# Optimization experiments

Measured on AMD Instinct MI355X. Metric: run time of the kernel, lower is better.

## Reference

```python
import jax, jax.numpy as jnp
import numpy as np
from jax.scipy.special import logsumexp

EPSILON = 0.1
MAX_ITERS = 20

B, S, T = 8, 2048, 2048


def setup_inputs() -> dict:
    key = jax.random.key(0)
    k1, k2, k3 = jax.random.split(key, 3)
    cost = jax.random.normal(k1, (B, S, T), dtype=jnp.float32)
    mu = jax.random.uniform(k2, (B, S), dtype=jnp.float32)
    nu = jax.random.uniform(k3, (B, T), dtype=jnp.float32)
    # normalize to probability distributions (realistic OT marginals)
    mu = mu / jnp.sum(mu, axis=-1, keepdims=True)
    nu = nu / jnp.sum(nu, axis=-1, keepdims=True)
    return {"cost": cost, "mu": mu, "nu": nu}


def reference(cost, mu, nu):
    tiny = jnp.finfo(cost.dtype).tiny
    log_mu = jnp.log(jnp.maximum(mu, tiny))          # (B, S)
    log_nu = jnp.log(jnp.maximum(nu, tiny))          # (B, T)
    log_K = -cost / EPSILON                          # (B, S, T)

    def step(carry, _):
        log_u, log_v = carry
        # row update: logsumexp over targets
        log_u = log_mu - logsumexp(log_K + log_v[:, None, :], axis=-1)  # (B, S)
        # col update: logsumexp over sources (equiv. to transpose in torch code)
        log_v = log_nu - logsumexp(log_K + log_u[:, :, None], axis=-2)  # (B, T)
        return (log_u, log_v), None

    init = (jnp.zeros_like(log_mu), jnp.zeros_like(log_nu))
    (log_u, log_v), _ = jax.lax.scan(step, init, None, length=MAX_ITERS)

    log_pi = log_u[:, :, None] + log_K + log_v[:, None, :]  # (B, S, T)
    transport = jnp.exp(log_pi)
    return transport, log_pi
```

## Files before the change

### kernel.cpp

```cpp
#include <hip/hip_runtime.h>
#include <hip/hip_fp16.h>
#include <math.h>

#define BB 8
#define SS 2048
#define TT 2048
#define ITERS 20
#define NEG_EPS_INV -10.0f
#define NWAVE 4
#define NCHUNK 4
#define ROWS 32
#define NTILE (SS / ROWS)
#define TINYF 1.17549435e-38f

typedef float vfloat4 __attribute__((ext_vector_type(4)));

__device__ __forceinline__ float4 fma4v(float a, float4 x, float4 y) {
    return make_float4(fmaf(a, x.x, y.x), fmaf(a, x.y, y.y),
                       fmaf(a, x.z, y.z), fmaf(a, x.w, y.w));
}
__device__ __forceinline__ float4 max4(float4 a, float4 b) {
    return make_float4(fmaxf(a.x, b.x), fmaxf(a.y, b.y),
                       fmaxf(a.z, b.z), fmaxf(a.w, b.w));
}
__device__ __forceinline__ float hmax4(float4 a) {
    return fmaxf(fmaxf(a.x, a.y), fmaxf(a.z, a.w));
}
__device__ __forceinline__ float hsum4(float4 a) {
    return (a.x + a.y) + (a.z + a.w);
}
__device__ __forceinline__ float4 exp4m(float4 x, float m) {
    return make_float4(__expf(x.x - m), __expf(x.y - m),
                       __expf(x.z - m), __expf(x.w - m));
}
__device__ __forceinline__ uint h2u(__half2 h) {
    union { __half2 h; uint u; } c; c.h = h; return c.u;
}
__device__ __forceinline__ __half2 u2h(uint u) {
    union { __half2 h; uint u; } c; c.u = u; return c.h;
}
__device__ __forceinline__ uint2 pack4(float4 f) {
    uint2 r;
    r.x = h2u(__float22half2_rn(make_float2(f.x, f.y)));
    r.y = h2u(__float22half2_rn(make_float2(f.z, f.w)));
    return r;
}
__device__ __forceinline__ float4 unpack4(uint2 u) {
    float2 a = __half22float2(u2h(u.x));
    float2 b = __half22float2(u2h(u.y));
    return make_float4(a.x, a.y, b.x, b.y);
}
__device__ __forceinline__ void nt_store4(float4 v, float* p) {
    vfloat4 x = {v.x, v.y, v.z, v.w};
    __builtin_nontemporal_store(x, reinterpret_cast<vfloat4*>(p));
}

template <bool FIRST>
__global__ __launch_bounds__(256, 3) void sinkhorn_iter(
        const float* __restrict__ cost, uint2* __restrict__ c16,
        const float* __restrict__ mu, const float* __restrict__ nu,
        float* __restrict__ log_u,
        const float* __restrict__ vin, float* __restrict__ vout,
        const float* __restrict__ Pin, float* __restrict__ Pout) {
    int t = threadIdx.x;
    int w = t >> 6, l = t & 63;
    int tile = blockIdx.x, b = blockIdx.y;

    __shared__ float4 vlds[512];
    __shared__ float4 acc[NWAVE][512];

#pragma unroll
    for (int j = 0; j < 2; ++j) {
        int g = j * 256 + t;
        float4 vn;
        if constexpr (FIRST) {
            vn = make_float4(0.f, 0.f, 0.f, 0.f);
        } else {
            const float4* P4 = (const float4*)Pin;
            float4 s = make_float4(0.f, 0.f, 0.f, 0.f);
#pragma unroll 8
            for (int p = 0; p < NTILE; ++p) {
                float4 q = P4[(size_t)(p * BB + b) * 512 + g];
                s.x += q.x; s.y += q.y; s.z += q.z; s.w += q.w;
            }
            float4 lvold = ((const float4*)(vin + (size_t)b * TT))[g];
            float4 nv = ((const float4*)(nu + (size_t)b * TT))[g];
            vn.x = __logf(fmaxf(nv.x, TINYF)) + lvold.x - __logf(fmaxf(s.x, TINYF));
            vn.y = __logf(fmaxf(nv.y, TINYF)) + lvold.y - __logf(fmaxf(s.y, TINYF));
            vn.z = __logf(fmaxf(nv.z, TINYF)) + lvold.z - __logf(fmaxf(s.z, TINYF));
            vn.w = __logf(fmaxf(nv.w, TINYF)) + lvold.w - __logf(fmaxf(s.w, TINYF));
        }
        vlds[g] = vn;
        if (tile == 0) ((float4*)(vout + (size_t)b * TT))[g] = vn;
    }
#pragma unroll
    for (int i = 0; i < 8; ++i) acc[w][i * 64 + l] = make_float4(0.f, 0.f, 0.f, 0.f);
    __syncthreads();

    float4 vv[8];
#pragma unroll
    for (int i = 0; i < 8; ++i) vv[i] = vlds[i * 64 + l];

#pragma unroll
    for (int c = 0; c < NCHUNK; ++c) {
        int r0 = tile * ROWS + c * (2 * NWAVE) + w * 2;
        size_t rowbase = (size_t)(b * SS + r0) * TT;

        float4 x0[8], x1[8];
        if constexpr (FIRST) {
            const float4* c4 = (const float4*)(cost + rowbase);
            uint2* cw = c16 + rowbase / 4;
#pragma unroll
            for (int i = 0; i < 8; ++i) x0[i] = c4[i * 64 + l];
#pragma unroll
            for (int i = 0; i < 8; ++i) x1[i] = c4[512 + i * 64 + l];
#pragma unroll
            for (int i = 0; i < 8; ++i) {
                cw[i * 64 + l] = pack4(x0[i]);
                cw[512 + i * 64 + l] = pack4(x1[i]);
            }
        } else {
            const uint2* cr = (const uint2*)c16 + rowbase / 4;
#pragma unroll
            for (int i = 0; i < 8; ++i) x0[i] = unpack4(cr[i * 64 + l]);
#pragma unroll
            for (int i = 0; i < 8; ++i) x1[i] = unpack4(cr[512 + i * 64 + l]);
        }
#pragma unroll
        for (int i = 0; i < 8; ++i) {
            x0[i] = fma4v(NEG_EPS_INV, x0[i], vv[i]);
            x1[i] = fma4v(NEG_EPS_INV, x1[i], vv[i]);
        }

        float4 a0 = x0[0], a1 = x1[0];
#pragma unroll
        for (int i = 1; i < 8; ++i) { a0 = max4(a0, x0[i]); a1 = max4(a1, x1[i]); }
        float m0 = hmax4(a0), m1 = hmax4(a1);
#pragma unroll
        for (int off = 1; off < 64; off <<= 1) {
            m0 = fmaxf(m0, __shfl_xor(m0, off));
            m1 = fmaxf(m1, __shfl_xor(m1, off));
        }

        float ps0 = 0.0f, ps1 = 0.0f;
#pragma unroll
        for (int i = 0; i < 8; ++i) {
            x0[i] = exp4m(x0[i], m0);
            x1[i] = exp4m(x1[i], m1);
            ps0 += hsum4(x0[i]);
            ps1 += hsum4(x1[i]);
        }
#pragma unroll
        for (int off = 1; off < 64; off <<= 1) {
            ps0 += __shfl_xor(ps0, off);
            ps1 += __shfl_xor(ps1, off);
        }

        float g0 = mu[b * SS + r0] / ps0;
        float g1 = mu[b * SS + r0 + 1] / ps1;
        if (l == 0) {
            log_u[b * SS + r0]     = __logf(fmaxf(g0, TINYF)) - m0;
            log_u[b * SS + r0 + 1] = __logf(fmaxf(g1, TINYF)) - m1;
        }

#pragma unroll
        for (int i = 0; i < 8; ++i) {
            float4 o = acc[w][i * 64 + l];
            o.x = fmaf(g0, x0[i].x, fmaf(g1, x1[i].x, o.x));
            o.y = fmaf(g0, x0[i].y, fmaf(g1, x1[i].y, o.y));
            o.z = fmaf(g0, x0[i].z, fmaf(g1, x1[i].z, o.z));
            o.w = fmaf(g0, x0[i].w, fmaf(g1, x1[i].w, o.w));
            acc[w][i * 64 + l] = o;
        }
    }
    __syncthreads();

    float4* P4o = (float4*)Pout + (size_t)(tile * BB + b) * 512;
#pragma unroll
    for (int j = 0; j < 2; ++j) {
        int g = j * 256 + t;
        float4 s0 = acc[0][g], s1 = acc[1][g], s2 = acc[2][g], s3 = acc[3][g];
        float4 o;
        o.x = (s0.x + s1.x) + (s2.x + s3.x);
        o.y = (s0.y + s1.y) + (s2.y + s3.y);
        o.z = (s0.z + s1.z) + (s2.z + s3.z);
        o.w = (s0.w + s1.w) + (s2.w + s3.w);
        P4o[g] = o;
    }
}

__global__ __launch_bounds__(256) void combine_final(
        const float* __restrict__ P, const float* __restrict__ nu,
        const float* __restrict__ vin, float* __restrict__ vout) {
    int i = blockIdx.x * 256 + threadIdx.x;
    int b = i >> 11, col = i & (TT - 1);
    float tot = 0.0f;
#pragma unroll 8
    for (int p = 0; p < NTILE; ++p) tot += P[(size_t)(p * BB + b) * TT + col];
    vout[i] = __logf(fmaxf(nu[i], TINYF)) + vin[i] - __logf(fmaxf(tot, TINYF));
}

__global__ __launch_bounds__(256) void finalize(const uint2* __restrict__ c16,
                                                const float* __restrict__ log_u,
                                                const float* __restrict__ log_v,
                                                float* __restrict__ transport,
                                                float* __restrict__ log_pi) {
    int i = blockIdx.x * 256 + threadIdx.x;
    int flat = i * 4;
    int row = flat >> 11;
    int t = flat & (TT - 1);
    int b = row >> 11;

    float lu = log_u[row];
    float4 lv = *reinterpret_cast<const float4*>(log_v + (size_t)b * TT + t);
    float4 c = unpack4(c16[((size_t)row * TT + t) / 4]);

    float4 lp;
    lp.x = fmaf(NEG_EPS_INV, c.x, lu + lv.x);
    lp.y = fmaf(NEG_EPS_INV, c.y, lu + lv.y);
    lp.z = fmaf(NEG_EPS_INV, c.z, lu + lv.z);
    lp.w = fmaf(NEG_EPS_INV, c.w, lu + lv.w);

    float4 tr;
    tr.x = __expf(lp.x);
    tr.y = __expf(lp.y);
    tr.z = __expf(lp.z);
    tr.w = __expf(lp.w);

    nt_store4(tr, transport + (size_t)row * TT + t);
    nt_store4(lp, log_pi + (size_t)row * TT + t);
}

extern "C" void kernel_launch(void* const* d_in, const int* in_sizes, int n_in,
                              void* d_out, int out_size, void* d_ws, size_t ws_size,
                              hipStream_t stream) {
    const float* cost = (const float*)d_in[0];
    const float* mu = (const float*)d_in[1];
    const float* nu = (const float*)d_in[2];

    float* out = (float*)d_out;
    float* transport = out;
    float* log_pi = out + (size_t)BB * SS * TT;

    float* ws = (float*)d_ws;
    float* log_u = ws;
    float* vA = ws + 16384;
    float* vB = ws + 32768;
    float* PA = ws + (1 << 20);
    float* PB = PA + NTILE * BB * TT;
    uint2* c16 = (uint2*)(ws + (1 << 23));

    hipLaunchKernelGGL((sinkhorn_iter<true>), dim3(NTILE, BB), dim3(256), 0, stream,
                       cost, c16, mu, nu, log_u, vB, vA, PB, PA);
    for (int it = 1; it < ITERS; ++it) {
        float* vin  = (it & 1) ? vA : vB;
        float* vout = (it & 1) ? vB : vA;
        float* Pin  = (it & 1) ? PA : PB;
        float* Pout = (it & 1) ? PB : PA;
        hipLaunchKernelGGL((sinkhorn_iter<false>), dim3(NTILE, BB), dim3(256), 0, stream,
                           cost, c16, mu, nu, log_u, vin, vout, Pin, Pout);
    }
    hipLaunchKernelGGL(combine_final, dim3(BB * TT / 256), dim3(256), 0, stream,
                       PB, nu, vB, vA);

    hipLaunchKernelGGL(finalize, dim3(BB * SS * TT / 4 / 256), dim3(256), 0, stream,
                       c16, log_u, vA, transport, log_pi);
}
```

Before: 579.0 us.

## Fuse Sinkhorn iterations into one persistent kernel with atomic grid barriers

Replaces the 20 per-iteration launches and the combine kernel with a single persistent kernel. Blocks atomically add their column partial sums into a per-iteration buffer and wait on an atomic counter instead of relaunching. Each block then rebuilds log_v in registers from the summed column totals. This removes launch overhead and the 64-way partial-sum reduction, but adds a memset, many atomic float adds, and spin-wait barriers that require all 512 blocks to be resident at once, otherwise the kernel deadlocks.

New measurement: 1.607 ms. 178% more time.

```diff
diff --git a/kernel.cpp b/kernel.cpp
--- a/kernel.cpp
+++ b/kernel.cpp
@@ -11,6 +11,7 @@
 #define NCHUNK 4
 #define ROWS 32
 #define NTILE (SS / ROWS)
+#define NBLK (NTILE * BB)
 #define TINYF 1.17549435e-38f
 
 typedef float vfloat4 __attribute__((ext_vector_type(4)));
@@ -54,150 +55,177 @@
     vfloat4 x = {v.x, v.y, v.z, v.w};
     __builtin_nontemporal_store(x, reinterpret_cast<vfloat4*>(p));
 }
-
-template <bool FIRST>
-__global__ __launch_bounds__(256, 3) void sinkhorn_iter(
+__device__ __forceinline__ float aload(const float* p) {
+    return __hip_atomic_load(p, __ATOMIC_RELAXED, __HIP_MEMORY_SCOPE_AGENT);
+}
+
+__global__ __launch_bounds__(256, 2) void sinkhorn_persist(
         const float* __restrict__ cost, uint2* __restrict__ c16,
         const float* __restrict__ mu, const float* __restrict__ nu,
-        float* __restrict__ log_u,
-        const float* __restrict__ vin, float* __restrict__ vout,
-        const float* __restrict__ Pin, float* __restrict__ Pout) {
+        float* __restrict__ log_u, float* __restrict__ vfinal,
+        float* __restrict__ S, int* __restrict__ cnt) {
     int t = threadIdx.x;
     int w = t >> 6, l = t & 63;
     int tile = blockIdx.x, b = blockIdx.y;
 
-    __shared__ float4 vlds[512];
     __shared__ float4 acc[NWAVE][512];
 
-#pragma unroll
-    for (int j = 0; j < 2; ++j) {
-        int g = j * 256 + t;
-        float4 vn;
-        if constexpr (FIRST) {
-            vn = make_float4(0.f, 0.f, 0.f, 0.f);
-        } else {
-            const float4* P4 = (const float4*)Pin;
-            float4 s = make_float4(0.f, 0.f, 0.f, 0.f);
-#pragma unroll 8
-            for (int p = 0; p < NTILE; ++p) {
-                float4 q = P4[(size_t)(p * BB + b) * 512 + g];
-                s.x += q.x; s.y += q.y; s.z += q.z; s.w += q.w;
-            }
-            float4 lvold = ((const float4*)(vin + (size_t)b * TT))[g];
-            float4 nv = ((const float4*)(nu + (size_t)b * TT))[g];
-            vn.x = __logf(fmaxf(nv.x, TINYF)) + lvold.x - __logf(fmaxf(s.x, TINYF));
-            vn.y = __logf(fmaxf(nv.y, TINYF)) + lvold.y - __logf(fmaxf(s.y, TINYF));
-            vn.z = __logf(fmaxf(nv.z, TINYF)) + lvold.z - __logf(fmaxf(s.z, TINYF));
-            vn.w = __logf(fmaxf(nv.w, TINYF)) + lvold.w - __logf(fmaxf(s.w, TINYF));
-        }
-        vlds[g] = vn;
-        if (tile == 0) ((float4*)(vout + (size_t)b * TT))[g] = vn;
+    const float4* nu4 = (const float4*)(nu + (size_t)b * TT);
+    float4 ln[8], vv[8];
+#pragma unroll
+    for (int i = 0; i < 8; ++i) {
+        float4 nv = nu4[i * 64 + l];
+        ln[i] = make_float4(__logf(fmaxf(nv.x, TINYF)), __logf(fmaxf(nv.y, TINYF)),
+                            __logf(fmaxf(nv.z, TINYF)), __logf(fmaxf(nv.w, TINYF)));
+        vv[i] = make_float4(0.f, 0.f, 0.f, 0.f);
     }
-#pragma unroll
-    for (int i = 0; i < 8; ++i) acc[w][i * 64 + l] = make_float4(0.f, 0.f, 0.f, 0.f);
-    __syncthreads();
-
-    float4 vv[8];
-#pragma unroll
-    for (int i = 0; i < 8; ++i) vv[i] = vlds[i * 64 + l];
-
-#pragma unroll
-    for (int c = 0; c < NCHUNK; ++c) {
-        int r0 = tile * ROWS + c * (2 * NWAVE) + w * 2;
-        size_t rowbase = (size_t)(b * SS + r0) * TT;
-
-        float4 x0[8], x1[8];
-        if constexpr (FIRST) {
-            const float4* c4 = (const float4*)(cost + rowbase);
-            uint2* cw = c16 + rowbase / 4;
-#pragma unroll
-            for (int i = 0; i < 8; ++i) x0[i] = c4[i * 64 + l];
-#pragma unroll
-            for (int i = 0; i < 8; ++i) x1[i] = c4[512 + i * 64 + l];
-#pragma unroll
-            for (int i = 0; i < 8; ++i) {
-                cw[i * 64 + l] = pack4(x0[i]);
-                cw[512 + i * 64 + l] = pack4(x1[i]);
-            }
-        } else {
-            const uint2* cr = (const uint2*)c16 + rowbase / 4;
-#pragma unroll
-            for (int i = 0; i < 8; ++i) x0[i] = unpack4(cr[i * 64 + l]);
-#pragma unroll
-            for (int i = 0; i < 8; ++i) x1[i] = unpack4(cr[512 + i * 64 + l]);
-        }
+
+    for (int k = 0; k < ITERS; ++k) {
+        if (k > 0) {
+            if (t == 0) {
+                while (__hip_atomic_load(&cnt[k - 1], __ATOMIC_ACQUIRE,
+                                         __HIP_MEMORY_SCOPE_AGENT) < NBLK)
+                    __builtin_amdgcn_s_sleep(32);
+            }
+            __syncthreads();
+            const float* Sp = S + (size_t)(k - 1) * (BB * TT) + (size_t)b * TT;
+#pragma unroll
+            for (int i = 0; i < 8; ++i) {
+                int col = (i * 64 + l) * 4;
+                float s0 = aload(Sp + col + 0);
+                float s1 = aload(Sp + col + 1);
+                float s2 = aload(Sp + col + 2);
+                float s3 = aload(Sp + col + 3);
+                vv[i].x = ln[i].x + vv[i].x - __logf(fmaxf(s0, TINYF));
+                vv[i].y = ln[i].y + vv[i].y - __logf(fmaxf(s1, TINYF));
+                vv[i].z = ln[i].z + vv[i].z - __logf(fmaxf(s2, TINYF));
+                vv[i].w = ln[i].w + vv[i].w - __logf(fmaxf(s3, TINYF));
+            }
+        }
+
+#pragma unroll
+        for (int i = 0; i < 8; ++i) acc[w][i * 64 + l] = make_float4(0.f, 0.f, 0.f, 0.f);
+
+#pragma unroll
+        for (int c = 0; c < NCHUNK; ++c) {
+            int r0 = tile * ROWS + c * (2 * NWAVE) + w * 2;
+            size_t rowbase = (size_t)(b * SS + r0) * TT;
+
+            float4 x0[8], x1[8];
+            if (k == 0) {
+                const float4* c4 = (const float4*)(cost + rowbase);
+                uint2* cw = c16 + rowbase / 4;
+#pragma unroll
+                for (int i = 0; i < 8; ++i) x0[i] = c4[i * 64 + l];
+#pragma unroll
+                for (int i = 0; i < 8; ++i) x1[i] = c4[512 + i * 64 + l];
+#pragma unroll
+                for (int i = 0; i < 8; ++i) {
+                    cw[i * 64 + l] = pack4(x0[i]);
+                    cw[512 + i * 64 + l] = pack4(x1[i]);
+                }
+            } else {
+                const uint2* cr = (const uint2*)c16 + rowbase / 4;
+#pragma unroll
+                for (int i = 0; i < 8; ++i) x0[i] = unpack4(cr[i * 64 + l]);
+#pragma unroll
+                for (int i = 0; i < 8; ++i) x1[i] = unpack4(cr[512 + i * 64 + l]);
+            }
+#pragma unroll
+            for (int i = 0; i < 8; ++i) {
+                x0[i] = fma4v(NEG_EPS_INV, x0[i], vv[i]);
+                x1[i] = fma4v(NEG_EPS_INV, x1[i], vv[i]);
+            }
+
+            float4 a0 = x0[0], a1 = x1[0];
+#pragma unroll
+            for (int i = 1; i < 8; ++i) { a0 = max4(a0, x0[i]); a1 = max4(a1, x1[i]); }
+            float m0 = hmax4(a0), m1 = hmax4(a1);
+#pragma unroll
+            for (int off = 1; off < 64; off <<= 1) {
+                m0 = fmaxf(m0, __shfl_xor(m0, off));
+                m1 = fmaxf(m1, __shfl_xor(m1, off));
+            }
+
+            float ps0 = 0.0f, ps1 = 0.0f;
+#pragma unroll
+            for (int i = 0; i < 8; ++i) {
+                x0[i] = exp4m(x0[i], m0);
+                x1[i] = exp4m(x1[i], m1);
+                ps0 += hsum4(x0[i]);
+                ps1 += hsum4(x1[i]);
+            }
+#pragma unroll
+            for (int off = 1; off < 64; off <<= 1) {
+                ps0 += __shfl_xor(ps0, off);
+                ps1 += __shfl_xor(ps1, off);
+            }
+
+            float g0 = mu[b * SS + r0] / ps0;
+            float g1 = mu[b * SS + r0 + 1] / ps1;
+            if (l == 0) {
+                log_u[b * SS + r0]     = __logf(fmaxf(g0, TINYF)) - m0;
+                log_u[b * SS + r0 + 1] = __logf(fmaxf(g1, TINYF)) - m1;
+            }
+
+#pragma unroll
+            for (int i = 0; i < 8; ++i) {
+                float4 o = acc[w][i * 64 + l];
+                o.x = fmaf(g0, x0[i].x, fmaf(g1, x1[i].x, o.x));
+                o.y = fmaf(g0, x0[i].y, fmaf(g1, x1[i].y, o.y));
+                o.z = fmaf(g0, x0[i].z, fmaf(g1, x1[i].z, o.z));
+                o.w = fmaf(g0, x0[i].w, fmaf(g1, x1[i].w, o.w));
+                acc[w][i * 64 + l] = o;
+            }
+        }
+        __syncthreads();
+
+        float* Sk = S + (size_t)k * (BB * TT) + (size_t)b * TT;
+#pragma unroll
+        for (int j = 0; j < 2; ++j) {
+            int g = j * 256 + t;
+            float4 s0 = acc[0][g], s1 = acc[1][g], s2 = acc[2][g], s3 = acc[3][g];
+            float4 s;
+            s.x = (s0.x + s1.x) + (s2.x + s3.x);
+            s.y = (s0.y + s1.y) + (s2.y + s3.y);
+            s.z = (s0.z + s1.z) + (s2.z + s3.z);
+            s.w = (s0.w + s1.w) + (s2.w + s3.w);
+            int col = g * 4;
+            unsafeAtomicAdd(Sk + col + 0, s.x);
+            unsafeAtomicAdd(Sk + col + 1, s.y);
+            unsafeAtomicAdd(Sk + col + 2, s.z);
+            unsafeAtomicAdd(Sk + col + 3, s.w);
+        }
+        __syncthreads();
+        if (t == 0)
+            __hip_atomic_fetch_add(&cnt[k], 1, __ATOMIC_RELEASE,
+                                   __HIP_MEMORY_SCOPE_AGENT);
+    }
+
+    if (tile == 0) {
+        if (t == 0) {
+            while (__hip_atomic_load(&cnt[ITERS - 1], __ATOMIC_ACQUIRE,
+                                     __HIP_MEMORY_SCOPE_AGENT) < NBLK)
+                __builtin_amdgcn_s_sleep(32);
+        }
+        __syncthreads();
+        const float* Sp = S + (size_t)(ITERS - 1) * (BB * TT) + (size_t)b * TT;
+        float4* vf4 = (float4*)(vfinal + (size_t)b * TT);
 #pragma unroll
         for (int i = 0; i < 8; ++i) {
-            x0[i] = fma4v(NEG_EPS_INV, x0[i], vv[i]);
-            x1[i] = fma4v(NEG_EPS_INV, x1[i], vv[i]);
-        }
-
-        float4 a0 = x0[0], a1 = x1[0];
-#pragma unroll
-        for (int i = 1; i < 8; ++i) { a0 = max4(a0, x0[i]); a1 = max4(a1, x1[i]); }
-        float m0 = hmax4(a0), m1 = hmax4(a1);
-#pragma unroll
-        for (int off = 1; off < 64; off <<= 1) {
-            m0 = fmaxf(m0, __shfl_xor(m0, off));
-            m1 = fmaxf(m1, __shfl_xor(m1, off));
-        }
-
-        float ps0 = 0.0f, ps1 = 0.0f;
-#pragma unroll
-        for (int i = 0; i < 8; ++i) {
-            x0[i] = exp4m(x0[i], m0);
-            x1[i] = exp4m(x1[i], m1);
-            ps0 += hsum4(x0[i]);
-            ps1 += hsum4(x1[i]);
-        }
-#pragma unroll
-        for (int off = 1; off < 64; off <<= 1) {
-            ps0 += __shfl_xor(ps0, off);
-            ps1 += __shfl_xor(ps1, off);
-        }
-
-        float g0 = mu[b * SS + r0] / ps0;
-        float g1 = mu[b * SS + r0 + 1] / ps1;
-        if (l == 0) {
-            log_u[b * SS + r0]     = __logf(fmaxf(g0, TINYF)) - m0;
-            log_u[b * SS + r0 + 1] = __logf(fmaxf(g1, TINYF)) - m1;
-        }
-
-#pragma unroll
-        for (int i = 0; i < 8; ++i) {
-            float4 o = acc[w][i * 64 + l];
-            o.x = fmaf(g0, x0[i].x, fmaf(g1, x1[i].x, o.x));
-            o.y = fmaf(g0, x0[i].y, fmaf(g1, x1[i].y, o.y));
-            o.z = fmaf(g0, x0[i].z, fmaf(g1, x1[i].z, o.z));
-            o.w = fmaf(g0, x0[i].w, fmaf(g1, x1[i].w, o.w));
-            acc[w][i * 64 + l] = o;
+            int col = (i * 64 + l) * 4;
+            float s0 = aload(Sp + col + 0);
+            float s1 = aload(Sp + col + 1);
+            float s2 = aload(Sp + col + 2);
+            float s3 = aload(Sp + col + 3);
+            float4 vn;
+            vn.x = ln[i].x + vv[i].x - __logf(fmaxf(s0, TINYF));
+            vn.y = ln[i].y + vv[i].y - __logf(fmaxf(s1, TINYF));
+            vn.z = ln[i].z + vv[i].z - __logf(fmaxf(s2, TINYF));
+            vn.w = ln[i].w + vv[i].w - __logf(fmaxf(s3, TINYF));
+            vf4[i * 64 + l] = vn;
         }
     }
-    __syncthreads();
-
-    float4* P4o = (float4*)Pout + (size_t)(tile * BB + b) * 512;
-#pragma unroll
-    for (int j = 0; j < 2; ++j) {
-        int g = j * 256 + t;
-        float4 s0 = acc[0][g], s1 = acc[1][g], s2 = acc[2][g], s3 = acc[3][g];
-        float4 o;
-        o.x = (s0.x + s1.x) + (s2.x + s3.x);
-        o.y = (s0.y + s1.y) + (s2.y + s3.y);
-        o.z = (s0.z + s1.z) + (s2.z + s3.z);
-        o.w = (s0.w + s1.w) + (s2.w + s3.w);
-        P4o[g] = o;
-    }
-}
-
-__global__ __launch_bounds__(256) void combine_final(
-        const float* __restrict__ P, const float* __restrict__ nu,
-        const float* __restrict__ vin, float* __restrict__ vout) {
-    int i = blockIdx.x * 256 + threadIdx.x;
-    int b = i >> 11, col = i & (TT - 1);
-    float tot = 0.0f;
-#pragma unroll 8
-    for (int p = 0; p < NTILE; ++p) tot += P[(size_t)(p * BB + b) * TT + col];
-    vout[i] = __logf(fmaxf(nu[i], TINYF)) + vin[i] - __logf(fmaxf(tot, TINYF));
 }
 
 __global__ __launch_bounds__(256) void finalize(const uint2* __restrict__ c16,
@@ -243,26 +271,17 @@
     float* log_pi = out + (size_t)BB * SS * TT;
 
     float* ws = (float*)d_ws;
-    float* log_u = ws;
-    float* vA = ws + 16384;
-    float* vB = ws + 32768;
-    float* PA = ws + (1 << 20);
-    float* PB = PA + NTILE * BB * TT;
+    int* cnt = (int*)ws;
+    float* log_u = ws + 1024;
+    float* vfinal = ws + 1024 + 16384;
+    float* S = ws + 65536;
     uint2* c16 = (uint2*)(ws + (1 << 23));
 
-    hipLaunchKernelGGL((sinkhorn_iter<true>), dim3(NTILE, BB), dim3(256), 0, stream,
-                       cost, c16, mu, nu, log_u, vB, vA, PB, PA);
-    for (int it = 1; it < ITERS; ++it) {
-        float* vin  = (it & 1) ? vA : vB;
-        float* vout = (it & 1) ? vB : vA;
-        float* Pin  = (it & 1) ? PA : PB;
-        float* Pout = (it & 1) ? PB : PA;
-        hipLaunchKernelGGL((sinkhorn_iter<false>), dim3(NTILE, BB), dim3(256), 0, stream,
-                           cost, c16, mu, nu, log_u, vin, vout, Pin, Pout);
-    }
-    hipLaunchKernelGGL(combine_final, dim3(BB * TT / 256), dim3(256), 0, stream,
-                       PB, nu, vB, vA);
+    hipMemsetAsync(ws, 0, (65536 + ITERS * BB * TT) * sizeof(float), stream);
+
+    hipLaunchKernelGGL(sinkhorn_persist, dim3(NTILE, BB), dim3(256), 0, stream,
+                       cost, c16, mu, nu, log_u, vfinal, S, cnt);
 
     hipLaunchKernelGGL(finalize, dim3(BB * SS * TT / 4 / 256), dim3(256), 0, stream,
-                       c16, log_u, vA, transport, log_pi);
-}
+                       c16, log_u, vfinal, transport, log_pi);
+}
```
